# Performance work log

Hardware: AMD Instinct MI355X
Metric: run time of the kernel (lower is better)

The kernel has to match this reference:

```python
import jax, jax.numpy as jnp
import numpy as np

B, C, CI, T, H, W = 4, 256, 128, 8, 28, 28
EPS = 1e-5


def setup_inputs() -> dict:
    key = jax.random.key(0)
    ks = jax.random.split(key, 12)
    s = 0.02
    return {
        "x": jax.random.normal(ks[0], (B, C, T, H, W), jnp.float32),
        "Wg": jax.random.normal(ks[1], (CI, C), jnp.float32) * s,
        "bg": jax.random.normal(ks[2], (CI,), jnp.float32) * s,
        "Wt": jax.random.normal(ks[3], (CI, C), jnp.float32) * s,
        "bt": jax.random.normal(ks[4], (CI,), jnp.float32) * s,
        "Wp": jax.random.normal(ks[5], (CI, C), jnp.float32) * s,
        "bp": jax.random.normal(ks[6], (CI,), jnp.float32) * s,
        "Ww": jax.random.normal(ks[7], (C, CI), jnp.float32) * s,
        "bw": jax.random.normal(ks[8], (C,), jnp.float32) * s,
        "gamma": jax.random.normal(ks[9], (C,), jnp.float32) * s + 1.0,
        "beta": jax.random.normal(ks[10], (C,), jnp.float32) * s,
        "rmean": jax.random.normal(ks[11], (C,), jnp.float32) * s,
        "rvar": jax.random.uniform(jax.random.fold_in(key, 99), (C,), jnp.float32, 0.5, 1.5),
    }


def reference(x, Wg, bg, Wt, bt, Wp, bp, Ww, bw, gamma, beta, rmean, rvar):
    b, c, t, h, w = x.shape
    n = t * h * w
    xf = x.reshape(b, c, n)                                   # [B,C,N]
    # 1x1x1 conv projections == per-position linear maps
    g = jnp.einsum('oc,bcn->bno', Wg, xf) + bg                # [B,N,Ci]
    th = jnp.einsum('oc,bcn->bno', Wt, xf) + bt               # [B,N,Ci]
    ph = jnp.einsum('oc,bcn->bon', Wp, xf) + bp[None, :, None]  # [B,Ci,N]
    f = jnp.einsum('bnc,bcm->bnm', th, ph)                    # [B,N,N] attention logits
    attn = jax.nn.softmax(f, axis=-1)
    y = jnp.einsum('bnm,bmo->bno', attn, g)                   # [B,N,Ci]
    wy = jnp.einsum('co,bno->bcn', Ww, y) + bw[None, :, None]  # [B,C,N]
    # BatchNorm3d (eval mode: running stats)
    inv = gamma / jnp.sqrt(rvar + EPS)
    wy = wy * inv[None, :, None] + (beta - rmean * inv)[None, :, None]
    z = wy + xf                                               # residual
    return z.reshape(b, c, t, h, w)
```

## Files before the change

### kernel.cpp

```cpp
#include <hip/hip_runtime.h>
#include <hip/hip_bf16.h>
#include <hip/hip_fp8.h>

#define BB 4
#define CC 256
#define CI 128
#define NN 6272
#define LOG2E 1.4426950408889634f

#define KSTRIDE 136
#define VSTRIDE 72
#define KBUF (64 * KSTRIDE)
#define VBUF (128 * VSTRIDE)

typedef __attribute__((ext_vector_type(8))) __bf16 bf16x8;
typedef __attribute__((ext_vector_type(4))) __bf16 bf16x4;
typedef __attribute__((ext_vector_type(4))) float f32x4;
typedef __attribute__((ext_vector_type(16))) float f32x16;

__device__ __forceinline__ unsigned cvtpk_fp8(float a, float b) {
  unsigned r;
  asm("v_cvt_pk_fp8_f32 %0, %1, %2" : "=v"(r) : "v"(a), "v"(b));
  return r;
}

__device__ __forceinline__ unsigned char to_fp8(float v) {
  __hip_fp8_e4m3 t(v);
  return *reinterpret_cast<unsigned char*>(&t);
}

__global__ void nlb_prep(const float* __restrict__ Wg, const float* __restrict__ bg,
                         const float* __restrict__ Wt, const float* __restrict__ bt,
                         const float* __restrict__ Wp, const float* __restrict__ bp,
                         const float* __restrict__ Ww, const float* __restrict__ bw,
                         const float* __restrict__ gamma, const float* __restrict__ beta,
                         const float* __restrict__ rmean, const float* __restrict__ rvar,
                         __bf16* __restrict__ wall, float* __restrict__ ball,
                         __bf16* __restrict__ wwb, float* __restrict__ scale,
                         float* __restrict__ shift) {
  int idx = blockIdx.x * 256 + threadIdx.x;
  if (idx < 384 * 256) {
    int o = idx >> 8, c = idx & 255;
    float v, bv;
    if (o < 128)      { v = Wt[o * 256 + c] * LOG2E;  bv = bt[o] * LOG2E; }
    else if (o < 256) { v = Wp[(o - 128) * 256 + c]; bv = bp[o - 128]; }
    else              { v = Wg[(o - 256) * 256 + c]; bv = bg[o - 256]; }
    wall[idx] = (__bf16)v;
    if (c == 0) ball[o] = bv;
  } else if (idx < 384 * 256 + 256 * 128) {
    int i = idx - 384 * 256;
    wwb[i] = (__bf16)Ww[i];
  } else if (idx < 384 * 256 + 256 * 128 + 256) {
    int c = idx - (384 * 256 + 256 * 128);
    float inv = gamma[c] * rsqrtf(rvar[c] + 1e-5f);
    scale[c] = inv;
    shift[c] = (bw[c] - rmean[c]) * inv + beta[c];
  }
}

__launch_bounds__(256)
__global__ void nlb_proj(const float* __restrict__ x, const __bf16* __restrict__ wall,
                         const float* __restrict__ ball,
                         unsigned char* __restrict__ Q8, unsigned char* __restrict__ K8,
                         unsigned char* __restrict__ V8t) {
  const int nb = blockIdx.x;
  const int b  = blockIdx.y;
  const int tid = threadIdx.x;
  const int lane = tid & 63, w = tid >> 6;
  const int n0 = nb * 64;
  const int r = lane & 15, g = lane >> 4;

  __shared__ __bf16 xl[64][40];

  const float* xb = x + (size_t)b * CC * NN;
  f32x4 acc[6][4] = {};

  const int snn = tid & 63;
  const int skg = tid >> 6;

  for (int k0 = 0; k0 < 256; k0 += 32) {
    bf16x8 tmp;
#pragma unroll
    for (int i = 0; i < 8; ++i)
      tmp[i] = (__bf16)xb[(size_t)(k0 + skg * 8 + i) * NN + n0 + snn];
    __syncthreads();
    *reinterpret_cast<bf16x8*>(&xl[snn][skg * 8]) = tmp;
    __syncthreads();

    bf16x8 bfrag[4];
#pragma unroll
    for (int j = 0; j < 4; ++j)
      bfrag[j] = *reinterpret_cast<const bf16x8*>(&xl[j * 16 + r][g * 8]);
#pragma unroll
    for (int mb = 0; mb < 6; ++mb) {
      bf16x8 afrag = *reinterpret_cast<const bf16x8*>(
          &wall[(size_t)(mb * 64 + w * 16 + r) * 256 + k0 + g * 8]);
#pragma unroll
      for (int j = 0; j < 4; ++j)
        acc[mb][j] = __builtin_amdgcn_mfma_f32_16x16x32_bf16(afrag, bfrag[j], acc[mb][j], 0, 0, 0);
    }
  }

#pragma unroll
  for (int mb = 0; mb < 6; ++mb) {
    const int m0 = mb * 64 + w * 16;
    if (m0 < 256) {
      unsigned char* dst = (m0 < 128) ? Q8 : K8;
      const int obase = (m0 < 128) ? m0 : (m0 - 128);
#pragma unroll
      for (int j = 0; j < 4; ++j) {
        int n = n0 + j * 16 + r;
        union { unsigned char bch[4]; unsigned u; } pk;
#pragma unroll
        for (int reg = 0; reg < 4; ++reg) {
          int o = m0 + g * 4 + reg;
          pk.bch[reg] = to_fp8(acc[mb][j][reg] + ball[o]);
        }
        *reinterpret_cast<unsigned*>(&dst[((size_t)b * NN + n) * CI + obase + g * 4]) = pk.u;
      }
    } else {
#pragma unroll
      for (int j = 0; j < 4; ++j) {
        int n = n0 + j * 16 + r;
#pragma unroll
        for (int reg = 0; reg < 4; ++reg) {
          int o = m0 + g * 4 + reg;
          float v = acc[mb][j][reg] + ball[o];
          V8t[((size_t)b * CI + (o - 256)) * NN + n] = to_fp8(v);
        }
      }
    }
  }
}

__launch_bounds__(256, 4)
__global__ void nlb_attn(const unsigned char* __restrict__ Q8,
                         const unsigned char* __restrict__ K8,
                         const unsigned char* __restrict__ V8t,
                         __bf16* __restrict__ Yp, float* __restrict__ Lp) {
  const int bid = blockIdx.x;
  const int pair = bid & 7;
  const int b  = pair >> 1, ks = pair & 1;
  const int qb = bid >> 3;
  const int tid = threadIdx.x, lane = tid & 63, w = tid >> 6;
  const int c = lane & 31, hi = lane >> 5;
  const int wq = w & 1, h = w >> 1;
  const int q0 = qb * 64 + wq * 32;
  const int NT = 49;

  const unsigned char* Qb = Q8  + (size_t)b * NN * CI;
  const char* Kb = (const char*)(K8 + (size_t)b * NN * CI);
  const char* Vb = (const char*)(V8t + (size_t)b * CI * NN);

  __shared__ __align__(16) char sm[2 * KBUF + 2 * VBUF];
  __shared__ float mls[2][64];

  uint4 gk0, gk1, gv0, gv1;
  const char* ksrc = Kb + (size_t)(ks * NT) * 8192 + tid * 32;
  const char* vsrc = Vb + (size_t)(tid >> 1) * NN + (ks * NT) * 64 + (tid & 1) * 32;
  auto gload = [&]() {
    gk0 = *reinterpret_cast<const uint4*>(ksrc);
    gk1 = *reinterpret_cast<const uint4*>(ksrc + 16);
    gv0 = *reinterpret_cast<const uint4*>(vsrc);
    gv1 = *reinterpret_cast<const uint4*>(vsrc + 16);
    ksrc += 8192; vsrc += 64;
  };
  char* const kd_base = sm + (tid >> 2) * KSTRIDE + (tid & 3) * 32;
  char* const vd_base = sm + 2 * KBUF + (tid >> 1) * VSTRIDE + (tid & 1) * 32;
  auto swrite = [&](int bb) {
    char* kd = kd_base + bb * KBUF;
    *reinterpret_cast<uint2*>(kd + 0)  = make_uint2(gk0.x, gk0.y);
    *reinterpret_cast<uint2*>(kd + 8)  = make_uint2(gk0.z, gk0.w);
    *reinterpret_cast<uint2*>(kd + 16) = make_uint2(gk1.x, gk1.y);
    *reinterpret_cast<uint2*>(kd + 24) = make_uint2(gk1.z, gk1.w);
    char* vd = vd_base + bb * VBUF;
    *reinterpret_cast<uint2*>(vd + 0)  = make_uint2(gv0.x, gv0.y);
    *reinterpret_cast<uint2*>(vd + 8)  = make_uint2(gv0.z, gv0.w);
    *reinterpret_cast<uint2*>(vd + 16) = make_uint2(gv1.x, gv1.y);
    *reinterpret_cast<uint2*>(vd + 24) = make_uint2(gv1.z, gv1.w);
  };

  long qf[8];
#pragma unroll
  for (int kc = 0; kc < 8; ++kc)
    qf[kc] = *reinterpret_cast<const long*>(&Qb[(size_t)(q0 + c) * CI + kc * 16 + hi * 8]);

  f32x16 yacc[4] = {};
  float l_acc = 0.f;

  gload();
  swrite(0);
  __syncthreads();

  int buf = 0;
  for (int t = 0; t < NT; ++t) {
    if (t + 1 < NT) gload();
    const char* kl = sm + buf * KBUF;
    const char* vl = sm + 2 * KBUF + buf * VBUF;

    f32x16 s;
#pragma unroll
    for (int i = 0; i < 16; ++i) s[i] = -4.f;
    __builtin_amdgcn_s_setprio(1);
#pragma unroll
    for (int kc = 0; kc < 8; ++kc) {
      long kf = *reinterpret_cast<const long*>(
          kl + (h * 32 + c) * KSTRIDE + kc * 16 + hi * 8);
      s = __builtin_amdgcn_mfma_f32_32x32x16_fp8_fp8(kf, qf[kc], s, 0, 0, 0);
    }
    __builtin_amdgcn_s_setprio(0);

#pragma unroll
    for (int reg = 0; reg < 16; ++reg) s[reg] = exp2f(s[reg]);
    float l0 = ((s[0] + s[1]) + (s[2] + s[3])) + ((s[4] + s[5]) + (s[6] + s[7]));
    float l1 = ((s[8] + s[9]) + (s[10] + s[11])) + ((s[12] + s[13]) + (s[14] + s[15]));
    l_acc += l0 + l1;

    unsigned pw[4];
#pragma unroll
    for (int i = 0; i < 4; ++i) {
      unsigned lo  = cvtpk_fp8(s[4 * i + 0], s[4 * i + 1]);
      unsigned hi2 = cvtpk_fp8(s[4 * i + 2], s[4 * i + 3]);
      pw[i] = __builtin_amdgcn_perm(hi2, lo, 0x05040100);
    }

    __builtin_amdgcn_s_setprio(1);
#pragma unroll
    for (int ch = 0; ch < 2; ++ch) {
      unsigned A = pw[ch * 2 + 0], B = pw[ch * 2 + 1];
      unsigned sX = (unsigned)__shfl_xor((int)(hi ? A : B), 32);
      unsigned plo = hi ? sX : A;
      unsigned phi = hi ? B : sX;
      long pa = (long)(((unsigned long long)phi << 32) | plo);
#pragma unroll
      for (int cb = 0; cb < 4; ++cb) {
        long vf = *reinterpret_cast<const long*>(
            vl + (cb * 32 + c) * VSTRIDE + h * 32 + ch * 16 + hi * 8);
        yacc[cb] = __builtin_amdgcn_mfma_f32_32x32x16_fp8_fp8(pa, vf, yacc[cb], 0, 0, 0);
      }
    }
    __builtin_amdgcn_s_setprio(0);

    if (t + 1 < NT) swrite(buf ^ 1);
    __syncthreads();
    buf ^= 1;
  }

  float l_full = l_acc + __shfl_xor(l_acc, 32);

  float* scr = (float*)sm;
  if (h == 1) {
    float* base = scr + wq * 4096;
#pragma unroll
    for (int cb = 0; cb < 4; ++cb)
#pragma unroll
      for (int reg = 0; reg < 16; ++reg)
        base[(cb * 16 + reg) * 64 + lane] = yacc[cb][reg];
    mls[wq][lane] = l_full;
  }
  __syncthreads();
  if (h == 0) {
    const float* base = scr + wq * 4096;
    float lsum = l_full + mls[wq][lane];
    if (hi == 0)
      Lp[(size_t)(ks * 4 + b) * NN + q0 + c] = lsum;
    __bf16* Yb = Yp + (size_t)(ks * 4 + b) * NN * CI;
#pragma unroll
    for (int cb = 0; cb < 4; ++cb) {
#pragma unroll
      for (int reg = 0; reg < 16; ++reg) {
        int qloc = (reg & 3) + 8 * (reg >> 2) + 4 * hi;
        float v = yacc[cb][reg] + base[(cb * 16 + reg) * 64 + lane];
        Yb[(size_t)(q0 + qloc) * CI + cb * 32 + c] = (__bf16)v;
      }
    }
  }
}

__launch_bounds__(256)
__global__ void nlb_out(const __bf16* __restrict__ Yp, const float* __restrict__ Lp,
                        const __bf16* __restrict__ wwb,
                        const float* __restrict__ scale, const float* __restrict__ shift,
                        const float* __restrict__ x, float* __restrict__ out) {
  const int nb = blockIdx.x;
  const int mb = blockIdx.y;
  const int b  = blockIdx.z;
  const int tid = threadIdx.x, lane = tid & 63, w = tid >> 6;
  const int r = lane & 15, g = lane >> 4;
  const int n0 = nb * 64, c0 = mb * 64 + w * 16;

  const __bf16* Y0 = Yp + (size_t)b * NN * CI;
  const __bf16* Y1 = Yp + (size_t)(4 + b) * NN * CI;
  f32x4 acc[4] = {};
#pragma unroll
  for (int k0 = 0; k0 < 128; k0 += 32) {
    bf16x8 af = *reinterpret_cast<const bf16x8*>(&wwb[(size_t)(c0 + r) * CI + k0 + g * 8]);
#pragma unroll
    for (int j = 0; j < 4; ++j) {
      size_t yoff = (size_t)(n0 + j * 16 + r) * CI + k0 + g * 8;
      bf16x8 bf0 = *reinterpret_cast<const bf16x8*>(&Y0[yoff]);
      acc[j] = __builtin_amdgcn_mfma_f32_16x16x32_bf16(af, bf0, acc[j], 0, 0, 0);
      bf16x8 bf1 = *reinterpret_cast<const bf16x8*>(&Y1[yoff]);
      acc[j] = __builtin_amdgcn_mfma_f32_16x16x32_bf16(af, bf1, acc[j], 0, 0, 0);
    }
  }
  const float* xb = x + (size_t)b * CC * NN;
  float* ob = out + (size_t)b * CC * NN;
#pragma unroll
  for (int j = 0; j < 4; ++j) {
    int n = n0 + j * 16 + r;
    float il = 1.f / (Lp[(size_t)b * NN + n] + Lp[(size_t)(4 + b) * NN + n]);
#pragma unroll
    for (int reg = 0; reg < 4; ++reg) {
      int cc = c0 + g * 4 + reg;
      size_t off = (size_t)cc * NN + n;
      ob[off] = acc[j][reg] * (il * scale[cc]) + shift[cc] + xb[off];
    }
  }
}

extern "C" void kernel_launch(void* const* d_in, const int* in_sizes, int n_in,
                              void* d_out, int out_size, void* d_ws, size_t ws_size,
                              hipStream_t stream) {
  (void)in_sizes; (void)n_in; (void)out_size; (void)ws_size;
  const float* x     = (const float*)d_in[0];
  const float* Wg    = (const float*)d_in[1];
  const float* bg    = (const float*)d_in[2];
  const float* Wt    = (const float*)d_in[3];
  const float* bt    = (const float*)d_in[4];
  const float* Wp    = (const float*)d_in[5];
  const float* bp    = (const float*)d_in[6];
  const float* Ww    = (const float*)d_in[7];
  const float* bw    = (const float*)d_in[8];
  const float* gamma = (const float*)d_in[9];
  const float* beta  = (const float*)d_in[10];
  const float* rmean = (const float*)d_in[11];
  const float* rvar  = (const float*)d_in[12];
  float* out = (float*)d_out;

  char* ws = (char*)d_ws;
  __bf16* wall = (__bf16*)(ws + 0);
  float*  ball = (float*)(ws + 196608);
  __bf16* wwb  = (__bf16*)(ws + 198144);
  float*  scl  = (float*)(ws + 263680);
  float*  shf  = (float*)(ws + 264704);
  unsigned char* Q8 = (unsigned char*)(ws + 265728);
  unsigned char* K8 = (unsigned char*)(ws + 3476992);
  unsigned char* V8 = (unsigned char*)(ws + 6688256);
  __bf16* Yp   = (__bf16*)(ws + 9899520);
  float*  Lp   = (float*)(ws + 22744576);

  nlb_prep<<<513, 256, 0, stream>>>(Wg, bg, Wt, bt, Wp, bp, Ww, bw, gamma, beta,
                                    rmean, rvar, wall, ball, wwb, scl, shf);
  nlb_proj<<<dim3(98, 4), 256, 0, stream>>>(x, wall, ball, Q8, K8, V8);
  nlb_attn<<<784, 256, 0, stream>>>(Q8, K8, V8, Yp, Lp);
  nlb_out<<<dim3(98, 4, 4), 256, 0, stream>>>(Yp, Lp, wwb, scl, shf, x, out);
}
```

Before: 195.7 us.

## Store K/V in MFMA fragment order and load directly to registers, dropping LDS staging

The projection kernel now writes K and V in a pre-swizzled layout matching the fp8 MFMA operand fragments, so each lane loads its fragment with one contiguous 8-byte global read. The attention kernel removes the shared-memory double buffer and per-tile barriers. Each wave now handles its own quarter of the key range, with fragments prefetched one tile ahead in registers. The QK reduction is split into two independent accumulators to shorten the dependency chain, and launch bounds drop to 2 blocks per SM. In exchange, K/V data is no longer shared between waves through LDS, which raises global/L2 traffic, and occupancy may fall.

```diff
diff --git a/kernel.cpp b/kernel.cpp
--- a/kernel.cpp
+++ b/kernel.cpp
@@ -8,13 +8,7 @@
 #define NN 6272
 #define LOG2E 1.4426950408889634f
 
-#define KSTRIDE 136
-#define VSTRIDE 72
-#define KBUF (64 * KSTRIDE)
-#define VBUF (128 * VSTRIDE)
-
 typedef __attribute__((ext_vector_type(8))) __bf16 bf16x8;
-typedef __attribute__((ext_vector_type(4))) __bf16 bf16x4;
 typedef __attribute__((ext_vector_type(4))) float f32x4;
 typedef __attribute__((ext_vector_type(16))) float f32x16;
 
@@ -61,8 +55,8 @@
 __launch_bounds__(256)
 __global__ void nlb_proj(const float* __restrict__ x, const __bf16* __restrict__ wall,
                          const float* __restrict__ ball,
-                         unsigned char* __restrict__ Q8, unsigned char* __restrict__ K8,
-                         unsigned char* __restrict__ V8t) {
+                         unsigned char* __restrict__ Q8, unsigned char* __restrict__ KF,
+                         unsigned char* __restrict__ VF) {
   const int nb = blockIdx.x;
   const int b  = blockIdx.y;
   const int tid = threadIdx.x;
@@ -101,120 +95,116 @@
     }
   }
 
+  unsigned char* KFb = KF + (size_t)b * NN * CI;
+  unsigned char* VFb = VF + (size_t)b * NN * CI;
 #pragma unroll
   for (int mb = 0; mb < 6; ++mb) {
     const int m0 = mb * 64 + w * 16;
-    if (m0 < 256) {
-      unsigned char* dst = (m0 < 128) ? Q8 : K8;
-      const int obase = (m0 < 128) ? m0 : (m0 - 128);
+    if (m0 < 128) {
 #pragma unroll
       for (int j = 0; j < 4; ++j) {
         int n = n0 + j * 16 + r;
         union { unsigned char bch[4]; unsigned u; } pk;
 #pragma unroll
+        for (int reg = 0; reg < 4; ++reg)
+          pk.bch[reg] = to_fp8(acc[mb][j][reg] + ball[m0 + g * 4 + reg]);
+        *reinterpret_cast<unsigned*>(&Q8[((size_t)b * NN + n) * CI + m0 + g * 4]) = pk.u;
+      }
+    } else if (m0 < 256) {
+      const int kc = (m0 - 128) >> 4;
+#pragma unroll
+      for (int j = 0; j < 4; ++j) {
+        int n = n0 + j * 16 + r;
+        union { unsigned char bch[4]; unsigned u; } pk;
+#pragma unroll
+        for (int reg = 0; reg < 4; ++reg)
+          pk.bch[reg] = to_fp8(acc[mb][j][reg] + ball[m0 + g * 4 + reg]);
+        *reinterpret_cast<unsigned*>(
+            &KFb[(size_t)(n >> 5) * 4096 + kc * 512 + (g >> 1) * 256 + (n & 31) * 8 + (g & 1) * 4]) = pk.u;
+      }
+    } else {
+#pragma unroll
+      for (int j = 0; j < 4; ++j) {
+        int n = n0 + j * 16 + r;
+        const int g32 = n >> 5, kl = n & 31;
+        const int ch = kl >> 4, khi = (kl >> 3) & 1, kb = kl & 7;
+#pragma unroll
         for (int reg = 0; reg < 4; ++reg) {
           int o = m0 + g * 4 + reg;
-          pk.bch[reg] = to_fp8(acc[mb][j][reg] + ball[o]);
-        }
-        *reinterpret_cast<unsigned*>(&dst[((size_t)b * NN + n) * CI + obase + g * 4]) = pk.u;
-      }
-    } else {
-#pragma unroll
-      for (int j = 0; j < 4; ++j) {
-        int n = n0 + j * 16 + r;
-#pragma unroll
-        for (int reg = 0; reg < 4; ++reg) {
-          int o = m0 + g * 4 + reg;
+          int ci = o - 256, cb = ci >> 5, cc = ci & 31;
           float v = acc[mb][j][reg] + ball[o];
-          V8t[((size_t)b * CI + (o - 256)) * NN + n] = to_fp8(v);
+          VFb[(size_t)g32 * 4096 + (ch * 4 + cb) * 512 + khi * 256 + cc * 8 + kb] = to_fp8(v);
         }
       }
     }
   }
 }
 
-__launch_bounds__(256, 4)
+__launch_bounds__(256, 2)
 __global__ void nlb_attn(const unsigned char* __restrict__ Q8,
-                         const unsigned char* __restrict__ K8,
-                         const unsigned char* __restrict__ V8t,
+                         const unsigned char* __restrict__ KF,
+                         const unsigned char* __restrict__ VF,
                          __bf16* __restrict__ Yp, float* __restrict__ Lp) {
   const int bid = blockIdx.x;
   const int pair = bid & 7;
-  const int b  = pair >> 1, ks = pair & 1;
+  const int b = pair >> 1, kqp = pair & 1;
   const int qb = bid >> 3;
   const int tid = threadIdx.x, lane = tid & 63, w = tid >> 6;
   const int c = lane & 31, hi = lane >> 5;
-  const int wq = w & 1, h = w >> 1;
+  const int wq = w & 1, kqh = w >> 1;
   const int q0 = qb * 64 + wq * 32;
-  const int NT = 49;
-
-  const unsigned char* Qb = Q8  + (size_t)b * NN * CI;
-  const char* Kb = (const char*)(K8 + (size_t)b * NN * CI);
-  const char* Vb = (const char*)(V8t + (size_t)b * CI * NN);
-
-  __shared__ __align__(16) char sm[2 * KBUF + 2 * VBUF];
+  const int kq = kqp * 2 + kqh;
+
+  const unsigned char* Qb = Q8 + (size_t)b * NN * CI;
+  const char* kfp = (const char*)(KF + (size_t)b * NN * CI) + (size_t)(kq * 49) * 4096;
+  const char* vfp = (const char*)(VF + (size_t)b * NN * CI) + (size_t)(kq * 49) * 4096;
+
+  __shared__ float scr[2][4096];
   __shared__ float mls[2][64];
-
-  uint4 gk0, gk1, gv0, gv1;
-  const char* ksrc = Kb + (size_t)(ks * NT) * 8192 + tid * 32;
-  const char* vsrc = Vb + (size_t)(tid >> 1) * NN + (ks * NT) * 64 + (tid & 1) * 32;
-  auto gload = [&]() {
-    gk0 = *reinterpret_cast<const uint4*>(ksrc);
-    gk1 = *reinterpret_cast<const uint4*>(ksrc + 16);
-    gv0 = *reinterpret_cast<const uint4*>(vsrc);
-    gv1 = *reinterpret_cast<const uint4*>(vsrc + 16);
-    ksrc += 8192; vsrc += 64;
-  };
-  char* const kd_base = sm + (tid >> 2) * KSTRIDE + (tid & 3) * 32;
-  char* const vd_base = sm + 2 * KBUF + (tid >> 1) * VSTRIDE + (tid & 1) * 32;
-  auto swrite = [&](int bb) {
-    char* kd = kd_base + bb * KBUF;
-    *reinterpret_cast<uint2*>(kd + 0)  = make_uint2(gk0.x, gk0.y);
-    *reinterpret_cast<uint2*>(kd + 8)  = make_uint2(gk0.z, gk0.w);
-    *reinterpret_cast<uint2*>(kd + 16) = make_uint2(gk1.x, gk1.y);
-    *reinterpret_cast<uint2*>(kd + 24) = make_uint2(gk1.z, gk1.w);
-    char* vd = vd_base + bb * VBUF;
-    *reinterpret_cast<uint2*>(vd + 0)  = make_uint2(gv0.x, gv0.y);
-    *reinterpret_cast<uint2*>(vd + 8)  = make_uint2(gv0.z, gv0.w);
-    *reinterpret_cast<uint2*>(vd + 16) = make_uint2(gv1.x, gv1.y);
-    *reinterpret_cast<uint2*>(vd + 24) = make_uint2(gv1.z, gv1.w);
-  };
 
   long qf[8];
 #pragma unroll
   for (int kc = 0; kc < 8; ++kc)
     qf[kc] = *reinterpret_cast<const long*>(&Qb[(size_t)(q0 + c) * CI + kc * 16 + hi * 8]);
 
+  long kf[8], vf[8];
+#pragma unroll
+  for (int kc = 0; kc < 8; ++kc)
+    kf[kc] = *reinterpret_cast<const long*>(kfp + kc * 512 + lane * 8);
+#pragma unroll
+  for (int i = 0; i < 8; ++i)
+    vf[i] = *reinterpret_cast<const long*>(vfp + i * 512 + lane * 8);
+
   f32x16 yacc[4] = {};
   float l_acc = 0.f;
 
-  gload();
-  swrite(0);
-  __syncthreads();
-
-  int buf = 0;
-  for (int t = 0; t < NT; ++t) {
-    if (t + 1 < NT) gload();
-    const char* kl = sm + buf * KBUF;
-    const char* vl = sm + 2 * KBUF + buf * VBUF;
-
-    f32x16 s;
-#pragma unroll
-    for (int i = 0; i < 16; ++i) s[i] = -4.f;
+  for (int t = 0; t < 49; ++t) {
+    f32x16 sA, sB;
+#pragma unroll
+    for (int i = 0; i < 16; ++i) { sA[i] = -4.f; sB[i] = 0.f; }
     __builtin_amdgcn_s_setprio(1);
 #pragma unroll
-    for (int kc = 0; kc < 8; ++kc) {
-      long kf = *reinterpret_cast<const long*>(
-          kl + (h * 32 + c) * KSTRIDE + kc * 16 + hi * 8);
-      s = __builtin_amdgcn_mfma_f32_32x32x16_fp8_fp8(kf, qf[kc], s, 0, 0, 0);
+    for (int kc = 0; kc < 4; ++kc) {
+      sA = __builtin_amdgcn_mfma_f32_32x32x16_fp8_fp8(kf[kc], qf[kc], sA, 0, 0, 0);
+      sB = __builtin_amdgcn_mfma_f32_32x32x16_fp8_fp8(kf[kc + 4], qf[kc + 4], sB, 0, 0, 0);
     }
     __builtin_amdgcn_s_setprio(0);
 
-#pragma unroll
-    for (int reg = 0; reg < 16; ++reg) s[reg] = exp2f(s[reg]);
-    float l0 = ((s[0] + s[1]) + (s[2] + s[3])) + ((s[4] + s[5]) + (s[6] + s[7]));
-    float l1 = ((s[8] + s[9]) + (s[10] + s[11])) + ((s[12] + s[13]) + (s[14] + s[15]));
-    l_acc += l0 + l1;
+    if (t < 48) {
+      kfp += 4096;
+#pragma unroll
+      for (int kc = 0; kc < 8; ++kc)
+        kf[kc] = *reinterpret_cast<const long*>(kfp + kc * 512 + lane * 8);
+    }
+
+    float s[16];
+    float ps = 0.f;
+#pragma unroll
+    for (int reg = 0; reg < 16; ++reg) {
+      s[reg] = exp2f(sA[reg] + sB[reg]);
+      ps += s[reg];
+    }
+    l_acc += ps;
 
     unsigned pw[4];
 #pragma unroll
@@ -233,24 +223,24 @@
       unsigned phi = hi ? B : sX;
       long pa = (long)(((unsigned long long)phi << 32) | plo);
 #pragma unroll
-      for (int cb = 0; cb < 4; ++cb) {
-        long vf = *reinterpret_cast<const long*>(
-            vl + (cb * 32 + c) * VSTRIDE + h * 32 + ch * 16 + hi * 8);
-        yacc[cb] = __builtin_amdgcn_mfma_f32_32x32x16_fp8_fp8(pa, vf, yacc[cb], 0, 0, 0);
-      }
+      for (int cb = 0; cb < 4; ++cb)
+        yacc[cb] = __builtin_amdgcn_mfma_f32_32x32x16_fp8_fp8(pa, vf[ch * 4 + cb], yacc[cb], 0, 0, 0);
     }
     __builtin_amdgcn_s_setprio(0);
 
-    if (t + 1 < NT) swrite(buf ^ 1);
-    __syncthreads();
-    buf ^= 1;
+    if (t < 48) {
+      vfp += 4096;
+#pragma unroll
+      for (int i = 0; i < 8; ++i)
+        vf[i] = *reinterpret_cast<const long*>(vfp + i * 512 + lane * 8);
+    }
   }
 
   float l_full = l_acc + __shfl_xor(l_acc, 32);
 
-  float* scr = (float*)sm;
-  if (h == 1) {
-    float* base = scr + wq * 4096;
+  __syncthreads();
+  if (kqh == 1) {
+    float* base = &scr[wq][0];
 #pragma unroll
     for (int cb = 0; cb < 4; ++cb)
 #pragma unroll
@@ -259,12 +249,12 @@
     mls[wq][lane] = l_full;
   }
   __syncthreads();
-  if (h == 0) {
-    const float* base = scr + wq * 4096;
+  if (kqh == 0) {
+    const float* base = &scr[wq][0];
     float lsum = l_full + mls[wq][lane];
     if (hi == 0)
-      Lp[(size_t)(ks * 4 + b) * NN + q0 + c] = lsum;
-    __bf16* Yb = Yp + (size_t)(ks * 4 + b) * NN * CI;
+      Lp[(size_t)(kqp * 4 + b) * NN + q0 + c] = lsum;
+    __bf16* Yb = Yp + (size_t)(kqp * 4 + b) * NN * CI;
 #pragma unroll
     for (int cb = 0; cb < 4; ++cb) {
 #pragma unroll
@@ -345,14 +335,14 @@
   float*  scl  = (float*)(ws + 263680);
   float*  shf  = (float*)(ws + 264704);
   unsigned char* Q8 = (unsigned char*)(ws + 265728);
-  unsigned char* K8 = (unsigned char*)(ws + 3476992);
-  unsigned char* V8 = (unsigned char*)(ws + 6688256);
+  unsigned char* KF = (unsigned char*)(ws + 3476992);
+  unsigned char* VF = (unsigned char*)(ws + 6688256);
   __bf16* Yp   = (__bf16*)(ws + 9899520);
   float*  Lp   = (float*)(ws + 22744576);
 
   nlb_prep<<<513, 256, 0, stream>>>(Wg, bg, Wt, bt, Wp, bp, Ww, bw, gamma, beta,
                                     rmean, rvar, wall, ball, wwb, scl, shf);
-  nlb_proj<<<dim3(98, 4), 256, 0, stream>>>(x, wall, ball, Q8, K8, V8);
-  nlb_attn<<<784, 256, 0, stream>>>(Q8, K8, V8, Yp, Lp);
+  nlb_proj<<<dim3(98, 4), 256, 0, stream>>>(x, wall, ball, Q8, KF, VF);
+  nlb_attn<<<784, 256, 0, stream>>>(Q8, KF, VF, Yp, Lp);
   nlb_out<<<dim3(98, 4, 4), 256, 0, stream>>>(Yp, Lp, wwb, scl, shf, x, out);
 }
```

Result: faster. 183.0 us (-6.5%).
